# Performance work log

Hardware: AMD Instinct MI355X
Metric: run time of the kernel (lower is better)

Reference implementation:

```python
import jax, jax.numpy as jnp
import numpy as np

B, S, D = 4, 2048, 1024

def setup_inputs() -> dict:
    key = jax.random.key(0)
    k1, k2, k3, k4 = jax.random.split(key, 4)
    scale = 1.0 / np.sqrt(D)
    x = jax.random.normal(k1, (B, S, D), dtype=jnp.float32)
    Wq = jax.random.normal(k2, (D, D), dtype=jnp.float32) * scale
    Wk = jax.random.normal(k3, (D, D), dtype=jnp.float32) * scale
    Wv = jax.random.normal(k4, (D, D), dtype=jnp.float32) * scale
    return {"x": x, "Wq": Wq, "Wk": Wk, "Wv": Wv}

def reference(x, Wq, Wk, Wv):
    # Linear projections (nn.Linear with bias=False computes x @ W.T)
    q = jnp.einsum('bsd,ed->bse', x, Wq)
    k = jnp.einsum('bsd,ed->bse', x, Wk)
    v = jnp.einsum('bsd,ed->bse', x, Wv)
    # HRR binding: circular convolution of k and v == elementwise product in FFT domain
    fq = jnp.fft.fft(q, axis=-1)
    fk = jnp.fft.fft(k, axis=-1)
    fv = jnp.fft.fft(v, axis=-1)
    # Causal associative memory: cumulative sum of bound key-value pairs over sequence
    mem = jnp.cumsum(fk * fv, axis=-2)  # [B, S, D] complex
    # Unbind with query via approximate inverse (complex conjugate of fft(q))
    out = jnp.fft.ifft(mem * jnp.conj(fq), axis=-1).real
    return out.astype(x.dtype)
```

## Files before the change

kernel.cpp:

```cpp
#include <hip/hip_runtime.h>

#define BB 4
#define SS 2048
#define DD 1024
#define MM 8192
#define CH 64
#define RR 32
#define PI_F 3.14159265358979323846f

typedef __attribute__((ext_vector_type(8))) short bf16x8;
typedef __attribute__((ext_vector_type(4))) float f32x4;

__device__ __forceinline__ unsigned short f2bf(float f) {
  unsigned int u = __float_as_uint(f);
  u = (u + 0x7FFFu + ((u >> 16) & 1u)) >> 16;
  return (unsigned short)u;
}
__device__ __forceinline__ float bf2f(unsigned short h) {
  return __uint_as_float(((unsigned int)h) << 16);
}

__global__ __launch_bounds__(256) void convert_bf16(
    const float* __restrict__ src, unsigned short* __restrict__ dst) {
  const long i = ((long)blockIdx.x * 256 + threadIdx.x) * 4;
  const float4 v = *(const float4*)&src[i];
  ushort4 o;
  o.x = f2bf(v.x); o.y = f2bf(v.y); o.z = f2bf(v.z); o.w = f2bf(v.w);
  *(ushort4*)&dst[i] = o;
}

__global__ __launch_bounds__(256) void convert_w(
    const float* __restrict__ Wq, const float* __restrict__ Wk,
    const float* __restrict__ Wv, unsigned short* __restrict__ dst) {
  const int z = blockIdx.y;
  const float* src = (z == 0) ? Wq : (z == 1) ? Wk : Wv;
  const long i = ((long)blockIdx.x * 256 + threadIdx.x) * 4;
  const float4 v = *(const float4*)&src[i];
  ushort4 o;
  o.x = f2bf(v.x); o.y = f2bf(v.y); o.z = f2bf(v.z); o.w = f2bf(v.w);
  *(ushort4*)&dst[(size_t)z * DD * DD + i] = o;
}

__device__ __forceinline__ void async16(const void* g, void* l) {
  __builtin_amdgcn_global_load_lds(
      (const __attribute__((address_space(1))) void*)g,
      (__attribute__((address_space(3))) void*)l, 16, 0, 0);
}

#define GW(n)  asm volatile("s_waitcnt vmcnt(" #n ")" ::: "memory")
#define BAR()  asm volatile("s_barrier" ::: "memory")
#define SB0()  __builtin_amdgcn_sched_barrier(0)

#define STA(buf, i, T) async16(xb + (size_t)(m0 + 32 * (i)) * DD + (T) * 64 + sOff, \
                               &Als[(buf) * 8192 + (i) * 2048 + slot8])
#define STB(buf, i, T) async16(W + (size_t)(n0 + 32 * (i)) * DD + (T) * 64 + sOff, \
                               &Bls[(buf) * 8192 + (i) * 2048 + slot8])
#define LDA(buf) { _Pragma("unroll") for (int mt = 0; mt < 4; ++mt) { \
    af[mt][0] = *(const bf16x8*)&Als[(buf) * 8192 + aRd + mt * 1024 + qoff0]; \
    af[mt][1] = *(const bf16x8*)&Als[(buf) * 8192 + aRd + mt * 1024 + qoff1]; } }
#define LDB(buf, nt, bank) { \
    bank[0] = *(const bf16x8*)&Bls[(buf) * 8192 + bRd + (nt) * 1024 + qoff0]; \
    bank[1] = *(const bf16x8*)&Bls[(buf) * 8192 + bRd + (nt) * 1024 + qoff1]; }
#define MMA(nt, bank) { __builtin_amdgcn_s_setprio(1); \
    _Pragma("unroll") for (int mt = 0; mt < 4; ++mt) { \
      acc[mt][nt] = __builtin_amdgcn_mfma_f32_16x16x32_bf16(af[mt][0], bank[0], acc[mt][nt], 0, 0, 0); \
      acc[mt][nt] = __builtin_amdgcn_mfma_f32_16x16x32_bf16(af[mt][1], bank[1], acc[mt][nt], 0, 0, 0); } \
    __builtin_amdgcn_s_setprio(0); }

__global__ __launch_bounds__(256, 2) void gemm_mfma(
    const unsigned short* __restrict__ xb,
    const unsigned short* __restrict__ Wb,
    float* __restrict__ outq, unsigned short* __restrict__ KV) {
  const int z = blockIdx.z;
  const unsigned short* W = Wb + (size_t)z * DD * DD;

  __shared__ unsigned short Als[2 * 8192];
  __shared__ unsigned short Bls[2 * 8192];

  const int tid  = threadIdx.x;
  const int lane = tid & 63;
  const int w    = tid >> 6;
  const int wm   = w >> 1;
  const int wn   = w & 1;
  const int fr   = lane & 15;
  const int kq   = lane >> 4;

  const int m0 = blockIdx.x * 128;
  const int n0 = blockIdx.y * 128;

  const int srow  = tid >> 3;
  const int sq    = (tid & 7) ^ (srow & 7);
  const int slot8 = tid * 8;
  const size_t sOff = (size_t)srow * DD + sq * 8;

  const int qoff0 = ((0 + kq) ^ (fr & 7)) * 8;
  const int qoff1 = ((4 + kq) ^ (fr & 7)) * 8;
  const int aRd = wm * 4096 + fr * 64;
  const int bRd = wn * 4096 + fr * 64;

  f32x4 acc[4][4] = {};
  bf16x8 af[4][2];
  bf16x8 bva[2], bvb[2];

  STA(0, 0, 0); STA(0, 1, 0); STA(0, 2, 0); STA(0, 3, 0);
  STB(0, 0, 0); STB(0, 1, 0); STB(0, 2, 0); STB(0, 3, 0);
  STA(1, 0, 1); STA(1, 1, 1); STA(1, 2, 1); STA(1, 3, 1);

  for (int T = 0; T < 14; ++T) {
    const int buf = T & 1;
    SB0(); GW(4); BAR();
    LDB(buf, 0, bva);
    LDA(buf);
    LDB(buf, 1, bvb);
    STB(buf ^ 1, 0, T + 1); STB(buf ^ 1, 1, T + 1);
    STB(buf ^ 1, 2, T + 1); STB(buf ^ 1, 3, T + 1);
    MMA(0, bva);
    MMA(1, bvb);
    SB0(); BAR();
    LDB(buf, 2, bva);
    LDB(buf, 3, bvb);
    STA(buf, 0, T + 2); STA(buf, 1, T + 2);
    STA(buf, 2, T + 2); STA(buf, 3, T + 2);
    MMA(2, bva);
    MMA(3, bvb);
  }
  SB0(); GW(4); BAR();
  LDB(0, 0, bva); LDA(0); LDB(0, 1, bvb);
  STB(1, 0, 15); STB(1, 1, 15); STB(1, 2, 15); STB(1, 3, 15);
  MMA(0, bva); MMA(1, bvb);
  SB0(); BAR();
  LDB(0, 2, bva); LDB(0, 3, bvb);
  MMA(2, bva); MMA(3, bvb);
  SB0(); GW(0); BAR();
  LDB(1, 0, bva); LDA(1); LDB(1, 1, bvb);
  MMA(0, bva); MMA(1, bvb);
  SB0(); BAR();
  LDB(1, 2, bva); LDB(1, 3, bvb);
  MMA(2, bva); MMA(3, bvb);

  const int col = lane & 15;
  const int r0  = (lane >> 4) * 4;
  const int mBase = m0 + wm * 64;
  const int nBase = n0 + wn * 64;
  if (z == 0) {
    #pragma unroll
    for (int mt = 0; mt < 4; ++mt)
      #pragma unroll
      for (int nt = 0; nt < 4; ++nt)
        #pragma unroll
        for (int r = 0; r < 4; ++r)
          outq[(size_t)(mBase + mt * 16 + r0 + r) * DD + nBase + nt * 16 + col] =
              acc[mt][nt][r];
  } else {
    unsigned short* Ck = KV + (size_t)(z - 1) * DD;
    #pragma unroll
    for (int mt = 0; mt < 4; ++mt)
      #pragma unroll
      for (int nt = 0; nt < 4; ++nt)
        #pragma unroll
        for (int r = 0; r < 4; ++r)
          Ck[(size_t)(mBase + mt * 16 + r0 + r) * 2048 + nBase + nt * 16 + col] =
              f2bf(acc[mt][nt][r]);
  }
}

__device__ __forceinline__ int pidx(int i) { return i + (i >> 6); }
#define BUFSZ 1040
__device__ __forceinline__ int pidx16(int i) { return i + (i >> 4); }
#define MEMSZ 546

__device__ __forceinline__ int rev4(int p) {
  unsigned r = __brev((unsigned)p) >> 22;
  return (int)(((r & 0x155u) << 1) | ((r & 0x2AAu) >> 1));
}

__host__ __device__ constexpr int clog2(int s) {
  return (s == 256) ? 8 : (s == 64) ? 6 : (s == 16) ? 4 : (s == 4) ? 2 : 0;
}

template <int S>
__device__ __forceinline__ void fwd_stage(float2 x[4], int t) {
  float c1 = 1.0f, s1 = 0.0f;
  if (S > 1) {
    const int j = t & (S - 1);
    __sincosf(-2.0f * PI_F * (float)j / (float)(4 * S), &s1, &c1);
  }
  const float c2 = c1 * c1 - s1 * s1, s2 = 2.0f * c1 * s1;
  const float c3 = c1 * c2 - s1 * s2, s3 = c1 * s2 + s1 * c2;
  const float Ar = x[0].x + x[2].x, Ai = x[0].y + x[2].y;
  const float Br = x[1].x + x[3].x, Bi = x[1].y + x[3].y;
  const float Cr = x[0].x - x[2].x, Ci = x[0].y - x[2].y;
  const float dr = x[1].x - x[3].x, di = x[1].y - x[3].y;
  const float y1r = Cr + di, y1i = Ci - dr;
  const float y2r = Ar - Br, y2i = Ai - Bi;
  const float y3r = Cr - di, y3i = Ci + dr;
  x[0] = make_float2(Ar + Br, Ai + Bi);
  x[1] = make_float2(y1r * c1 - y1i * s1, y1r * s1 + y1i * c1);
  x[2] = make_float2(y2r * c2 - y2i * s2, y2r * s2 + y2i * c2);
  x[3] = make_float2(y3r * c3 - y3i * s3, y3r * s3 + y3i * c3);
}

template <int S>
__device__ __forceinline__ void inv_stage(float2 x[4], int t) {
  float c1 = 1.0f, s1 = 0.0f;
  if (S > 1) {
    const int j = t & (S - 1);
    __sincosf(2.0f * PI_F * (float)j / (float)(4 * S), &s1, &c1);
  }
  const float c2 = c1 * c1 - s1 * s1, s2 = 2.0f * c1 * s1;
  const float c3 = c1 * c2 - s1 * s2, s3 = c1 * s2 + s1 * c2;
  const float u0r = x[0].x,                   u0i = x[0].y;
  const float u1r = x[1].x * c1 - x[1].y * s1, u1i = x[1].x * s1 + x[1].y * c1;
  const float u2r = x[2].x * c2 - x[2].y * s2, u2i = x[2].x * s2 + x[2].y * c2;
  const float u3r = x[3].x * c3 - x[3].y * s3, u3i = x[3].x * s3 + x[3].y * c3;
  const float Er = u0r + u2r, Ei = u0i + u2i;
  const float Fr = u0r - u2r, Fi = u0i - u2i;
  const float Gr = u1r + u3r, Gi = u1i + u3i;
  const float Hr = u1r - u3r, Hi = u1i - u3i;
  x[0] = make_float2(Er + Gr, Ei + Gi);
  x[1] = make_float2(Fr - Hi, Fi + Hr);
  x[2] = make_float2(Er - Gr, Ei - Gi);
  x[3] = make_float2(Fr + Hi, Fi - Hr);
}

template <int SW, int SR>
__device__ __forceinline__ void xchg(float2* buf, float2 x[4], int t) {
  constexpr int LW2 = clog2(SW), LR = clog2(SR);
  #pragma unroll
  for (int n = 0; n < 4; ++n)
    buf[pidx(((t >> LW2) << (LW2 + 2)) + (t & (SW - 1)) + n * SW)] = x[n];
  __syncthreads();
  #pragma unroll
  for (int n = 0; n < 4; ++n)
    x[n] = buf[pidx(((t >> LR) << (LR + 2)) + (t & (SR - 1)) + n * SR)];
  __syncthreads();
}

__device__ __forceinline__ void fwd_fft(float2* buf, float2 x[4], int t) {
  fwd_stage<256>(x, t); xchg<256, 64>(buf, x, t);
  fwd_stage<64>(x, t);  xchg<64, 16>(buf, x, t);
  fwd_stage<16>(x, t);  xchg<16, 4>(buf, x, t);
  fwd_stage<4>(x, t);   xchg<4, 1>(buf, x, t);
  fwd_stage<1>(x, t);
  #pragma unroll
  for (int n = 0; n < 4; ++n) buf[pidx(4 * t + n)] = x[n];
  __syncthreads();
}

__global__ __launch_bounds__(256) void bind_kernel(unsigned short* __restrict__ KV) {
  __shared__ float2 buf[BUFSZ];
  const int t = threadIdx.x;
  unsigned short* row = KV + (long)blockIdx.x * 2048;

  float2 x[4];
  #pragma unroll
  for (int n = 0; n < 4; ++n) {
    const int i = t + 256 * n;
    x[n] = make_float2(bf2f(row[i]), bf2f(row[1024 + i]));
  }
  fwd_fft(buf, x, t);

  float2* Prow = (float2*)row;
  #pragma unroll
  for (int m = 0; m < 2; ++m) {
    const int s = t + 256 * m;
    if (s == 0) {
      const float2 W0   = buf[pidx(0)];
      const float2 W512 = buf[pidx(2)];
      Prow[0] = make_float2(W0.x * W0.y, W512.x * W512.y);
    } else {
      const int p1 = rev4(s);
      const int p2 = rev4(1024 - s);
      const float2 F1 = buf[pidx(p1)], F2 = buf[pidx(p2)];
      const float fkr = 0.5f * (F1.x + F2.x), fki = 0.5f * (F1.y - F2.y);
      const float fvr = 0.5f * (F1.y + F2.y), fvi = 0.5f * (F2.x - F1.x);
      Prow[s] = make_float2(fkr * fvr - fki * fvi, fkr * fvi + fki * fvr);
    }
  }
}

__global__ __launch_bounds__(256) void scan_chunk_sum(
    const float2* __restrict__ P, float2* __restrict__ csum) {
  const int chunk = blockIdx.x;
  const int batch = blockIdx.y >> 1;
  const int f = (blockIdx.y & 1) * 256 + threadIdx.x;
  long base = ((long)batch * SS + (long)chunk * RR) * 512 + f;
  float sr = 0.0f, si = 0.0f;
  #pragma unroll
  for (int i0 = 0; i0 < RR; i0 += 8) {
    float2 p[8];
    #pragma unroll
    for (int j = 0; j < 8; ++j) p[j] = P[base + (long)(i0 + j) * 512];
    #pragma unroll
    for (int j = 0; j < 8; ++j) { sr += p[j].x; si += p[j].y; }
  }
  csum[((long)batch * CH + chunk) * 512 + f] = make_float2(sr, si);
}

__global__ __launch_bounds__(256) void scan_chunk_scan(float2* csum) {
  const int col   = blockIdx.x * 4 + (threadIdx.x >> 6);
  const int batch = col >> 9;
  const int f     = col & 511;
  const int c     = threadIdx.x & 63;
  const long idx  = ((long)batch * CH + c) * 512 + f;
  const float2 v  = csum[idx];
  float rr = v.x, ri = v.y;
  #pragma unroll
  for (int d = 1; d < 64; d <<= 1) {
    const float ox = __shfl_up(rr, d);
    const float oy = __shfl_up(ri, d);
    if (c >= d) { rr += ox; ri += oy; }
  }
  float ex = __shfl_up(rr, 1);
  float ey = __shfl_up(ri, 1);
  if (c == 0) { ex = 0.0f; ey = 0.0f; }
  csum[idx] = make_float2(ex, ey);
}

__global__ __launch_bounds__(256) void scan_apply(
    float2* __restrict__ P, const float2* __restrict__ csum) {
  const int chunk = blockIdx.x;
  const int batch = blockIdx.y >> 1;
  const int f = (blockIdx.y & 1) * 256 + threadIdx.x;
  float2 off = csum[((long)batch * CH + chunk) * 512 + f];
  float ar = off.x, ai = off.y;
  long base = ((long)batch * SS + (long)chunk * RR) * 512 + f;
  #pragma unroll
  for (int i0 = 0; i0 < RR; i0 += 8) {
    float2 p[8];
    #pragma unroll
    for (int j = 0; j < 8; ++j) p[j] = P[base + (long)(i0 + j) * 512];
    #pragma unroll
    for (int j = 0; j < 8; ++j) {
      ar += p[j].x; ai += p[j].y;
      P[base + (long)(i0 + j) * 512] = make_float2(ar, ai);
    }
  }
}

__global__ __launch_bounds__(256) void unbind_kernel(
    float* __restrict__ qout, const float2* __restrict__ mem) {
  __shared__ float2 buf[BUFSZ];
  __shared__ float2 m0s[MEMSZ], m1s[MEMSZ];
  const int t = threadIdx.x;
  const long r0 = (long)blockIdx.x * 2;
  float* row0 = qout + r0 * DD;
  float* row1 = row0 + DD;
  const float2* mem0 = mem + r0 * 512;
  const float2* mem1 = mem0 + 512;

  float2 x[4];
  #pragma unroll
  for (int n = 0; n < 4; ++n) {
    const int i = t + 256 * n;
    x[n] = make_float2(row0[i], row1[i]);
  }
  #pragma unroll
  for (int n = 0; n < 2; ++n) {
    const int s = t + 256 * n;
    const float2 a = mem0[s], b = mem1[s];
    if (s == 0) {
      m0s[pidx16(0)]   = make_float2(a.x, 0.0f);
      m0s[pidx16(512)] = make_float2(a.y, 0.0f);
      m1s[pidx16(0)]   = make_float2(b.x, 0.0f);
      m1s[pidx16(512)] = make_float2(b.y, 0.0f);
    } else {
      m0s[pidx16(s)] = a;
      m1s[pidx16(s)] = b;
    }
  }
  fwd_fft(buf, x, t);

  float2 z[4];
  #pragma unroll
  for (int m = 0; m < 4; ++m) {
    const int p   = t + 256 * m;
    const int bin = rev4(p);
    const int p2  = rev4((1024 - bin) & 1023);
    const float2 F1 = buf[pidx(p)], F2 = buf[pidx(p2)];
    const float q0r = 0.5f * (F1.x + F2.x), q0i = 0.5f * (F1.y - F2.y);
    const float q1r = 0.5f * (F1.y + F2.y), q1i = 0.5f * (F2.x - F1.x);
    const int  ix = (bin <= 512) ? bin : 1024 - bin;
    const float sg = (bin <= 512) ? 1.0f : -1.0f;
    float2 m0 = m0s[pidx16(ix)], m1 = m1s[pidx16(ix)];
    m0.y *= sg; m1.y *= sg;
    const float z0r = m0.x * q0r + m0.y * q0i, z0i = m0.y * q0r - m0.x * q0i;
    const float z1r = m1.x * q1r + m1.y * q1i, z1i = m1.y * q1r - m1.x * q1i;
    z[m] = make_float2(z0r - z1i, z0i + z1r);
  }
  __syncthreads();
  #pragma unroll
  for (int m = 0; m < 4; ++m) buf[pidx(t + 256 * m)] = z[m];
  __syncthreads();
  #pragma unroll
  for (int n = 0; n < 4; ++n) x[n] = buf[pidx(4 * t + n)];

  inv_stage<1>(x, t);   xchg<1, 4>(buf, x, t);
  inv_stage<4>(x, t);   xchg<4, 16>(buf, x, t);
  inv_stage<16>(x, t);  xchg<16, 64>(buf, x, t);
  inv_stage<64>(x, t);  xchg<64, 256>(buf, x, t);
  inv_stage<256>(x, t);

  const float sc = 1.0f / 1024.0f;
  #pragma unroll
  for (int n = 0; n < 4; ++n) {
    const int i = t + 256 * n;
    row0[i] = x[n].x * sc;
    row1[i] = x[n].y * sc;
  }
}

extern "C" void kernel_launch(void* const* d_in, const int* in_sizes, int n_in,
                              void* d_out, int out_size, void* d_ws, size_t ws_size,
                              hipStream_t stream) {
  (void)in_sizes; (void)n_in; (void)out_size;
  const float* x  = (const float*)d_in[0];
  const float* Wq = (const float*)d_in[1];
  const float* Wk = (const float*)d_in[2];
  const float* Wv = (const float*)d_in[3];
  float* out = (float*)d_out;

  const size_t wbytes = (size_t)3 * DD * DD * 2;
  auto need = [&](size_t MHr, size_t nB) {
    return wbytes + MHr * DD * 2 + MHr * 4096 + nB * CH * 512 * 8;
  };
  const int nPass = (ws_size >= need(8192, 4)) ? 1 : 2;
  const size_t MH = MM / nPass;
  const int    nB = BB / nPass;

  char* ws = (char*)d_ws;
  unsigned short* Wb = (unsigned short*)ws;
  unsigned short* xb = (unsigned short*)(ws + wbytes);
  unsigned short* KV = (unsigned short*)(ws + wbytes + MH * DD * 2);
  float2*       csum = (float2*)((char*)KV + MH * 4096);

  convert_w<<<dim3(DD * DD / 1024, 3), 256, 0, stream>>>(Wq, Wk, Wv, Wb);

  for (int h = 0; h < nPass; ++h) {
    const float* xh   = x   + (size_t)h * MH * DD;
    float*       outh = out + (size_t)h * MH * DD;

    convert_bf16<<<MH * DD / 1024, 256, 0, stream>>>(xh, xb);
    gemm_mfma<<<dim3(MH / 128, DD / 128, 3), dim3(256), 0, stream>>>(xb, Wb, outh, KV);
    bind_kernel<<<MH, 256, 0, stream>>>(KV);
    scan_chunk_sum<<<dim3(CH, nB * 2), 256, 0, stream>>>((const float2*)KV, csum);
    scan_chunk_scan<<<nB * 128, 256, 0, stream>>>(csum);
    scan_apply<<<dim3(CH, nB * 2), 256, 0, stream>>>((float2*)KV, csum);
    unbind_kernel<<<MH / 2, 256, 0, stream>>>(outh, (const float2*)KV);
  }
}
```

Measured before the change: 225.5 us.

## Run bind FFT per wavefront with radix-16 register passes instead of block-wide stages

The bind kernel now assigns one 1024-point FFT row to each 64-lane wavefront, four rows per block, instead of one row per 256-thread block. Each lane holds 16 points and does two radix-4 stages in registers between LDS exchanges, using XOR-swizzled addressing and lgkmcnt waits in place of __syncthreads. This is meant to remove block-wide barriers and cut the number of LDS round trips. In exchange it raises register pressure and relies on wave-synchronous LDS ordering.

```diff
diff --git a/kernel.cpp b/kernel.cpp
--- a/kernel.cpp
+++ b/kernel.cpp
@@ -178,6 +178,23 @@
   return (s == 256) ? 8 : (s == 64) ? 6 : (s == 16) ? 4 : (s == 4) ? 2 : 0;
 }
 
+__device__ __forceinline__ void bf4(float2& a, float2& b, float2& c, float2& d,
+                                    float c1, float s1) {
+  const float c2 = c1 * c1 - s1 * s1, s2 = 2.0f * c1 * s1;
+  const float c3 = c1 * c2 - s1 * s2, s3 = c1 * s2 + s1 * c2;
+  const float Ar = a.x + c.x, Ai = a.y + c.y;
+  const float Br = b.x + d.x, Bi = b.y + d.y;
+  const float Cr = a.x - c.x, Ci = a.y - c.y;
+  const float dr = b.x - d.x, di = b.y - d.y;
+  const float y1r = Cr + di, y1i = Ci - dr;
+  const float y2r = Ar - Br, y2i = Ai - Bi;
+  const float y3r = Cr - di, y3i = Ci + dr;
+  a = make_float2(Ar + Br, Ai + Bi);
+  b = make_float2(y1r * c1 - y1i * s1, y1r * s1 + y1i * c1);
+  c = make_float2(y2r * c2 - y2i * s2, y2r * s2 + y2i * c2);
+  d = make_float2(y3r * c3 - y3i * s3, y3r * s3 + y3i * c3);
+}
+
 template <int S>
 __device__ __forceinline__ void fwd_stage(float2 x[4], int t) {
   float c1 = 1.0f, s1 = 0.0f;
@@ -185,19 +202,7 @@
     const int j = t & (S - 1);
     __sincosf(-2.0f * PI_F * (float)j / (float)(4 * S), &s1, &c1);
   }
-  const float c2 = c1 * c1 - s1 * s1, s2 = 2.0f * c1 * s1;
-  const float c3 = c1 * c2 - s1 * s2, s3 = c1 * s2 + s1 * c2;
-  const float Ar = x[0].x + x[2].x, Ai = x[0].y + x[2].y;
-  const float Br = x[1].x + x[3].x, Bi = x[1].y + x[3].y;
-  const float Cr = x[0].x - x[2].x, Ci = x[0].y - x[2].y;
-  const float dr = x[1].x - x[3].x, di = x[1].y - x[3].y;
-  const float y1r = Cr + di, y1i = Ci - dr;
-  const float y2r = Ar - Br, y2i = Ai - Bi;
-  const float y3r = Cr - di, y3i = Ci + dr;
-  x[0] = make_float2(Ar + Br, Ai + Bi);
-  x[1] = make_float2(y1r * c1 - y1i * s1, y1r * s1 + y1i * c1);
-  x[2] = make_float2(y2r * c2 - y2i * s2, y2r * s2 + y2i * c2);
-  x[3] = make_float2(y3r * c3 - y3i * s3, y3r * s3 + y3i * c3);
+  bf4(x[0], x[1], x[2], x[3], c1, s1);
 }
 
 template <int S>
@@ -247,31 +252,94 @@
   __syncthreads();
 }
 
+#define LKW() asm volatile("s_waitcnt lgkmcnt(0)" ::: "memory")
+
 __global__ __launch_bounds__(256) void bind_kernel(unsigned short* __restrict__ KV) {
-  __shared__ float2 buf[BUFSZ];
-  const int t = threadIdx.x;
-  unsigned short* row = KV + (long)blockIdx.x * 2048;
-
-  float2 x[4];
-  #pragma unroll
-  for (int n = 0; n < 4; ++n) {
-    const int i = t + 256 * n;
-    x[n] = make_float2(bf2f(row[i]), bf2f(row[1024 + i]));
-  }
-  fwd_fft(buf, x, t);
+  __shared__ float2 rbufs[4][BUFSZ];
+  const int l  = threadIdx.x & 63;
+  const int wv = threadIdx.x >> 6;
+  float2* rbuf = rbufs[wv];
+  unsigned short* row = KV + ((long)blockIdx.x * 4 + wv) * 2048;
+
+  float2 x[16];
+  #pragma unroll
+  for (int j = 0; j < 16; ++j) {
+    const int n = l + 64 * j;
+    x[j] = make_float2(bf2f(row[n]), bf2f(row[1024 + n]));
+  }
+
+  #pragma unroll
+  for (int b = 0; b < 4; ++b) {
+    float s1, c1;
+    __sincosf(-2.0f * PI_F * (float)(l + 64 * b) / 1024.0f, &s1, &c1);
+    bf4(x[b], x[b + 4], x[b + 8], x[b + 12], c1, s1);
+  }
+  {
+    float s1, c1;
+    __sincosf(-2.0f * PI_F * (float)l / 256.0f, &s1, &c1);
+    #pragma unroll
+    for (int b = 0; b < 4; ++b)
+      bf4(x[4 * b], x[4 * b + 1], x[4 * b + 2], x[4 * b + 3], c1, s1);
+  }
+
+  #pragma unroll
+  for (int j = 0; j < 16; ++j)
+    rbuf[(l ^ ((j & 3) << 2)) + 64 * j] = x[j];
+  LKW();
+  const int g = l >> 2, cc = l & 3;
+  #pragma unroll
+  for (int j = 0; j < 16; ++j) {
+    const int q = 64 * g + cc + 4 * j;
+    x[j] = rbuf[q ^ (((q >> 6) & 3) << 2)];
+  }
+
+  #pragma unroll
+  for (int b = 0; b < 4; ++b) {
+    float s1, c1;
+    __sincosf(-2.0f * PI_F * (float)(cc + 4 * b) / 64.0f, &s1, &c1);
+    bf4(x[b], x[b + 4], x[b + 8], x[b + 12], c1, s1);
+  }
+  {
+    float s1, c1;
+    __sincosf(-2.0f * PI_F * (float)cc / 16.0f, &s1, &c1);
+    #pragma unroll
+    for (int b = 0; b < 4; ++b)
+      bf4(x[4 * b], x[4 * b + 1], x[4 * b + 2], x[4 * b + 3], c1, s1);
+  }
+
+  #pragma unroll
+  for (int j = 0; j < 16; ++j) {
+    const int q = 64 * g + cc + 4 * j;
+    rbuf[q ^ ((q >> 4) & 15)] = x[j];
+  }
+  LKW();
+  #pragma unroll
+  for (int i = 0; i < 16; ++i) {
+    const int q = 16 * l + i;
+    x[i] = rbuf[q ^ ((q >> 4) & 15)];
+  }
+
+  #pragma unroll
+  for (int b = 0; b < 4; ++b)
+    bf4(x[4 * b], x[4 * b + 1], x[4 * b + 2], x[4 * b + 3], 1.0f, 0.0f);
+
+  #pragma unroll
+  for (int i = 0; i < 16; ++i)
+    rbuf[pidx(16 * l + i)] = x[i];
+  LKW();
 
   float2* Prow = (float2*)row;
   #pragma unroll
-  for (int m = 0; m < 2; ++m) {
-    const int s = t + 256 * m;
+  for (int m = 0; m < 8; ++m) {
+    const int s = l + 64 * m;
     if (s == 0) {
-      const float2 W0   = buf[pidx(0)];
-      const float2 W512 = buf[pidx(2)];
+      const float2 W0   = rbuf[pidx(0)];
+      const float2 W512 = rbuf[pidx(2)];
       Prow[0] = make_float2(W0.x * W0.y, W512.x * W512.y);
     } else {
       const int p1 = rev4(s);
       const int p2 = rev4(1024 - s);
-      const float2 F1 = buf[pidx(p1)], F2 = buf[pidx(p2)];
+      const float2 F1 = rbuf[pidx(p1)], F2 = rbuf[pidx(p2)];
       const float fkr = 0.5f * (F1.x + F2.x), fki = 0.5f * (F1.y - F2.y);
       const float fvr = 0.5f * (F1.y + F2.y), fvi = 0.5f * (F2.x - F1.x);
       Prow[s] = make_float2(fkr * fvr - fki * fvi, fkr * fvi + fki * fvr);
@@ -442,7 +510,7 @@
 
     convert_bf16<<<MH * DD / 1024, 256, 0, stream>>>(xh, xb);
     gemm_mfma<<<dim3(MH / 128, DD / 128, 3), dim3(256), 0, stream>>>(xb, Wb, outh, KV);
-    bind_kernel<<<MH, 256, 0, stream>>>(KV);
+    bind_kernel<<<MH / 4, 256, 0, stream>>>(KV);
     scan_chunk_sum<<<dim3(CH, nB * 2), 256, 0, stream>>>((const float2*)KV, csum);
     scan_chunk_scan<<<nB * 128, 256, 0, stream>>>(csum);
     scan_apply<<<dim3(CH, nB * 2), 256, 0, stream>>>((float2*)KV, csum);
```

Measured after the change: 220.6 us. 2.1% less time.
